# Kernel tuning notes

Hardware: AMD Instinct MI355X
Metric: run time of the kernel (lower is better)

Reference implementation:

```python
import jax, jax.numpy as jnp
import numpy as np
from jax import lax

B, S, H, I, E, K = 4, 4096, 1024, 3584, 8, 2


def setup_inputs() -> dict:
    key = jax.random.key(0)
    ks = jax.random.split(key, 5)
    scale_h = 1.0 / np.sqrt(H)
    scale_i = 1.0 / np.sqrt(I)
    return {
        "hidden_states": jax.random.normal(ks[0], (B, S, H), dtype=jnp.float32),
        "gate_w": jax.random.normal(ks[1], (E, H), dtype=jnp.float32) * scale_h,
        "w1": jax.random.normal(ks[2], (E, H, I), dtype=jnp.float32) * scale_h,
        "w3": jax.random.normal(ks[3], (E, H, I), dtype=jnp.float32) * scale_h,
        "w2": jax.random.normal(ks[4], (E, I, H), dtype=jnp.float32) * scale_i,
        "top_k": K,
    }


def reference(hidden_states, gate_w, w1, w3, w2, top_k):
    b, s, h = hidden_states.shape
    n_experts = gate_w.shape[0]
    x = hidden_states.reshape(-1, h)  # [T, H]

    # Router: softmax in fp32, top-k, renormalize (Mixtral style)
    logits = x @ gate_w.T  # [T, E]
    probs = jax.nn.softmax(logits.astype(jnp.float32), axis=-1)
    top_w, top_idx = lax.top_k(probs, top_k)  # [T, K]
    top_w = top_w.astype(x.dtype)
    top_w = top_w / jnp.sum(top_w, axis=-1, keepdims=True)

    # Per-token, per-expert combine weight: [T, E]
    one_hot = jax.nn.one_hot(top_idx, n_experts, dtype=x.dtype)  # [T, K, E]
    w_full = jnp.einsum("tk,tke->te", top_w, one_hot)

    out = jnp.zeros_like(x)
    for e in range(n_experts):  # fixed small loop over experts
        hidden = jax.nn.silu(x @ w1[e]) * (x @ w3[e])  # SwiGLU, [T, I]
        y = hidden @ w2[e]  # [T, H]
        out = out + y * w_full[:, e:e + 1]
    return out.reshape(b, s, h)
```

## Files before the change

kernel.cpp:

```cpp
#include <hip/hip_runtime.h>
#include <hip/hip_bf16.h>

#define T_TOK 16384
#define H_DIM 1024
#define I_DIM 3584
#define E_NUM 8
#define TOTP  32768

typedef __attribute__((ext_vector_type(8))) short s16x8;
typedef __attribute__((ext_vector_type(4))) float f32x4;
typedef unsigned short u16;

__device__ __forceinline__ u16 f2bf(float f) {
    union { float f; unsigned u; } c; c.f = f;
    unsigned r = c.u + 0x7fffu + ((c.u >> 16) & 1u);
    return (u16)(r >> 16);
}

__device__ __forceinline__ void glds16(const u16* g, u16* l) {
    __builtin_amdgcn_global_load_lds(
        (const __attribute__((address_space(1))) unsigned int*)g,
        (__attribute__((address_space(3))) unsigned int*)l,
        16, 0, 0);
}

__global__ __launch_bounds__(64)
void router_k(const float* __restrict__ x, const float* __restrict__ gw,
              int* __restrict__ tk_idx, float* __restrict__ tk_w,
              int* __restrict__ counts)
{
    int t = blockIdx.x;
    int lane = threadIdx.x;
    const float* xr = x + (size_t)t * H_DIM;
    float xv[16];
#pragma unroll
    for (int j = 0; j < 16; j++) xv[j] = xr[j * 64 + lane];
    float lg[E_NUM];
#pragma unroll
    for (int e = 0; e < E_NUM; e++) {
        const float* g = gw + e * H_DIM;
        float s = 0.f;
#pragma unroll
        for (int j = 0; j < 16; j++) s += xv[j] * g[j * 64 + lane];
#pragma unroll
        for (int off = 32; off > 0; off >>= 1) s += __shfl_xor(s, off, 64);
        lg[e] = s;
    }
    if (lane == 0) {
        int i1 = 0; float m1 = lg[0];
#pragma unroll
        for (int e = 1; e < E_NUM; e++) if (lg[e] > m1) { m1 = lg[e]; i1 = e; }
        int i2 = -1; float m2 = -3.4e38f;
#pragma unroll
        for (int e = 0; e < E_NUM; e++) if (e != i1 && lg[e] > m2) { m2 = lg[e]; i2 = e; }
        float p1 = 1.f / (1.f + __expf(m2 - m1));
        float p2 = 1.f - p1;
        tk_idx[t * 2]     = i1;
        tk_idx[t * 2 + 1] = i2;
        tk_w[t * 2]       = p1;
        tk_w[t * 2 + 1]   = p2;
        atomicAdd(&counts[i1], 1);
        atomicAdd(&counts[i2], 1);
    }
}

__global__ void offsets_k(const int* __restrict__ counts, int* __restrict__ offsets,
                          int* __restrict__ cursor)
{
    if (threadIdx.x == 0 && blockIdx.x == 0) {
        int acc = 0;
        for (int e = 0; e < E_NUM; e++) { offsets[e] = acc; cursor[e] = acc; acc += counts[e]; }
        offsets[E_NUM] = acc;
    }
}

__global__ __launch_bounds__(256)
void scatter_k(const int* __restrict__ tk_idx, const float* __restrict__ tk_w,
               int* __restrict__ cursor, int* __restrict__ perm, float* __restrict__ pw)
{
    int t = blockIdx.x * 256 + threadIdx.x;
    if (t >= T_TOK) return;
#pragma unroll
    for (int k = 0; k < 2; k++) {
        int e = tk_idx[t * 2 + k];
        int pos = atomicAdd(&cursor[e], 1);
        perm[pos] = t;
        pw[pos]   = tk_w[t * 2 + k];
    }
}

__global__ __launch_bounds__(256)
void cvt_x_k(const float* __restrict__ x, u16* __restrict__ xb)
{
    size_t i = ((size_t)blockIdx.x * 256 + threadIdx.x) * 8;
    float4 a = *reinterpret_cast<const float4*>(x + i);
    float4 b = *reinterpret_cast<const float4*>(x + i + 4);
    union { u16 s[8]; uint4 v; } u;
    u.s[0] = f2bf(a.x); u.s[1] = f2bf(a.y); u.s[2] = f2bf(a.z); u.s[3] = f2bf(a.w);
    u.s[4] = f2bf(b.x); u.s[5] = f2bf(b.y); u.s[6] = f2bf(b.z); u.s[7] = f2bf(b.w);
    *reinterpret_cast<uint4*>(xb + i) = u.v;
}

__global__ __launch_bounds__(256)
void tcvt_k(const float* __restrict__ src, u16* __restrict__ dst, int M, int N)
{
    size_t eo = (size_t)blockIdx.z * M * N;
    __shared__ u16 tl[32][33];
    int t = threadIdx.x;
    int r = t >> 3, c = (t & 7) * 4;
    int m0 = blockIdx.y * 32, n0 = blockIdx.x * 32;
    float4 v = *reinterpret_cast<const float4*>(src + eo + (size_t)(m0 + r) * N + n0 + c);
    tl[c + 0][r] = f2bf(v.x); tl[c + 1][r] = f2bf(v.y);
    tl[c + 2][r] = f2bf(v.z); tl[c + 3][r] = f2bf(v.w);
    __syncthreads();
    union { u16 s[4]; unsigned long long v; } u;
    u.s[0] = tl[r][c]; u.s[1] = tl[r][c + 1]; u.s[2] = tl[r][c + 2]; u.s[3] = tl[r][c + 3];
    *reinterpret_cast<unsigned long long*>(dst + eo + (size_t)(n0 + r) * M + m0 + c) = u.v;
}

__global__ __launch_bounds__(256, 2)
void gemm1_k(const u16* __restrict__ xb, const u16* __restrict__ w1t,
             const u16* __restrict__ w3t, const int* __restrict__ offsets,
             const int* __restrict__ perm, u16* __restrict__ hidden)
{
    int e = blockIdx.z;
    int base = offsets[e];
    int cnt  = offsets[e + 1] - base;
    int m0 = blockIdx.y * 128;
    if (m0 >= cnt) return;
    int n0 = blockIdx.x * 64;

    __shared__ u16 As[128 * 32];
    __shared__ u16 B1s[64 * 32];
    __shared__ u16 B3s[64 * 32];

    int t = threadIdx.x;
    int lane = t & 63, wave = t >> 6;
    int wm = (wave >> 1) * 64, wn = (wave & 1) * 32;
    int l15 = lane & 15, quad = lane >> 4;

    int sr = t >> 2;
    int sc = (t & 3) * 8;
    int p0 = m0 + sr;      if (p0 > cnt - 1) p0 = cnt - 1;
    int p1 = m0 + 64 + sr; if (p1 > cnt - 1) p1 = cnt - 1;
    const u16* a0p = xb + (size_t)perm[base + p0] * H_DIM + sc;
    const u16* a1p = xb + (size_t)perm[base + p1] * H_DIM + sc;
    const u16* b1p = w1t + (size_t)e * I_DIM * H_DIM + (size_t)(n0 + sr) * H_DIM + sc;
    const u16* b3p = w3t + (size_t)e * I_DIM * H_DIM + (size_t)(n0 + sr) * H_DIM + sc;

    u16* As0 = As + t * 8;
    u16* As1 = As + 2048 + t * 8;
    u16* B1d = B1s + t * 8;
    u16* B3d = B3s + t * 8;

    f32x4 acc1[4][2] = {};
    f32x4 acc3[4][2] = {};

    for (int k0 = 0; k0 < H_DIM; k0 += 32) {
        glds16(a0p + k0, As0);
        glds16(a1p + k0, As1);
        glds16(b1p + k0, B1d);
        glds16(b3p + k0, B3d);
        __syncthreads();
        s16x8 af[4];
#pragma unroll
        for (int i = 0; i < 4; i++)
            af[i] = *reinterpret_cast<const s16x8*>(As + (wm + i * 16 + l15) * 32 + quad * 8);
#pragma unroll
        for (int j = 0; j < 2; j++) {
            s16x8 b1 = *reinterpret_cast<const s16x8*>(B1s + (wn + j * 16 + l15) * 32 + quad * 8);
            s16x8 b3 = *reinterpret_cast<const s16x8*>(B3s + (wn + j * 16 + l15) * 32 + quad * 8);
#pragma unroll
            for (int i = 0; i < 4; i++) {
                acc1[i][j] = __builtin_amdgcn_mfma_f32_16x16x32_bf16(af[i], b1, acc1[i][j], 0, 0, 0);
                acc3[i][j] = __builtin_amdgcn_mfma_f32_16x16x32_bf16(af[i], b3, acc3[i][j], 0, 0, 0);
            }
        }
        __syncthreads();
    }

#pragma unroll
    for (int i = 0; i < 4; i++) {
#pragma unroll
        for (int j = 0; j < 2; j++) {
            int col = n0 + wn + j * 16 + l15;
#pragma unroll
            for (int r = 0; r < 4; r++) {
                int p = m0 + wm + i * 16 + quad * 4 + r;
                if (p < cnt) {
                    float z1 = acc1[i][j][r];
                    float z3 = acc3[i][j][r];
                    float hv = (z1 / (1.f + __expf(-z1))) * z3;
                    hidden[(size_t)(base + p) * I_DIM + col] = f2bf(hv);
                }
            }
        }
    }
}

__global__ __launch_bounds__(256, 2)
void gemm2_k(const u16* __restrict__ hidden, const u16* __restrict__ w2t,
             const int* __restrict__ offsets, const int* __restrict__ perm,
             const float* __restrict__ pw, float* __restrict__ out)
{
    int e = blockIdx.z;
    int base = offsets[e];
    int cnt  = offsets[e + 1] - base;
    int m0 = blockIdx.y * 128;
    if (m0 >= cnt) return;
    int n0 = blockIdx.x * 128;

    __shared__ u16 As[128 * 32];
    __shared__ u16 Bs[128 * 32];

    int t = threadIdx.x;
    int lane = t & 63, wave = t >> 6;
    int wm = (wave >> 1) * 64, wn = (wave & 1) * 64;
    int l15 = lane & 15, quad = lane >> 4;

    int sr = t >> 2;
    int sc = (t & 3) * 8;
    int p0 = m0 + sr;      if (p0 > cnt - 1) p0 = cnt - 1;
    int p1 = m0 + 64 + sr; if (p1 > cnt - 1) p1 = cnt - 1;
    const u16* a0p = hidden + (size_t)(base + p0) * I_DIM + sc;
    const u16* a1p = hidden + (size_t)(base + p1) * I_DIM + sc;
    const u16* wb  = w2t + (size_t)e * H_DIM * I_DIM;
    const u16* b0p = wb + (size_t)(n0 + sr) * I_DIM + sc;
    const u16* b1p = wb + (size_t)(n0 + 64 + sr) * I_DIM + sc;

    u16* As0 = As + t * 8;
    u16* As1 = As + 2048 + t * 8;
    u16* Bs0 = Bs + t * 8;
    u16* Bs1 = Bs + 2048 + t * 8;

    f32x4 acc[4][4] = {};

    for (int k0 = 0; k0 < I_DIM; k0 += 32) {
        glds16(a0p + k0, As0);
        glds16(a1p + k0, As1);
        glds16(b0p + k0, Bs0);
        glds16(b1p + k0, Bs1);
        __syncthreads();
        s16x8 af[4];
#pragma unroll
        for (int i = 0; i < 4; i++)
            af[i] = *reinterpret_cast<const s16x8*>(As + (wm + i * 16 + l15) * 32 + quad * 8);
#pragma unroll
        for (int j = 0; j < 4; j++) {
            s16x8 bfv = *reinterpret_cast<const s16x8*>(Bs + (wn + j * 16 + l15) * 32 + quad * 8);
#pragma unroll
            for (int i = 0; i < 4; i++)
                acc[i][j] = __builtin_amdgcn_mfma_f32_16x16x32_bf16(af[i], bfv, acc[i][j], 0, 0, 0);
        }
        __syncthreads();
    }

#pragma unroll
    for (int i = 0; i < 4; i++) {
#pragma unroll
        for (int r = 0; r < 4; r++) {
            int p = m0 + wm + i * 16 + quad * 4 + r;
            if (p < cnt) {
                int tok = perm[base + p];
                float wgt = pw[base + p];
                float* orow = out + (size_t)tok * H_DIM + n0 + wn;
#pragma unroll
                for (int j = 0; j < 4; j++)
                    atomicAdd(orow + j * 16 + l15, wgt * acc[i][j][r]);
            }
        }
    }
}

extern "C" void kernel_launch(void* const* d_in, const int* in_sizes, int n_in,
                              void* d_out, int out_size, void* d_ws, size_t ws_size,
                              hipStream_t stream)
{
    (void)in_sizes; (void)n_in; (void)ws_size;
    const float* x  = (const float*)d_in[0];
    const float* gw = (const float*)d_in[1];
    const float* w1 = (const float*)d_in[2];
    const float* w3 = (const float*)d_in[3];
    const float* w2 = (const float*)d_in[4];
    float* out = (float*)d_out;

    char* ws = (char*)d_ws;
    int*   counts  = (int*)ws;
    int*   offsets = counts + 8;
    int*   cursor  = offsets + 9;
    int*   tk_idx  = (int*)(ws + 128);
    float* tk_w    = (float*)(ws + 128 + 131072);
    int*   perm    = (int*)(ws + 128 + 2 * 131072);
    float* pw      = (float*)(ws + 128 + 3 * 131072);
    u16* xb     = (u16*)(ws + (1 << 20));
    u16* w1t    = xb + 16777216ull;
    u16* w3t    = w1t + 29360128ull;
    u16* w2t    = w3t + 29360128ull;
    u16* hidden = w2t + 29360128ull;

    hipMemsetAsync(ws, 0, 128, stream);
    router_k<<<T_TOK, 64, 0, stream>>>(x, gw, tk_idx, tk_w, counts);
    offsets_k<<<1, 64, 0, stream>>>(counts, offsets, cursor);
    scatter_k<<<T_TOK / 256, 256, 0, stream>>>(tk_idx, tk_w, cursor, perm, pw);
    cvt_x_k<<<8192, 256, 0, stream>>>(x, xb);
    tcvt_k<<<dim3(I_DIM / 32, H_DIM / 32, E_NUM), 256, 0, stream>>>(w1, w1t, H_DIM, I_DIM);
    tcvt_k<<<dim3(I_DIM / 32, H_DIM / 32, E_NUM), 256, 0, stream>>>(w3, w3t, H_DIM, I_DIM);
    tcvt_k<<<dim3(H_DIM / 32, I_DIM / 32, E_NUM), 256, 0, stream>>>(w2, w2t, I_DIM, H_DIM);
    gemm1_k<<<dim3(I_DIM / 64, 128, E_NUM), 256, 0, stream>>>(xb, w1t, w3t, offsets, perm, hidden);
    hipMemsetAsync(out, 0, (size_t)out_size * sizeof(float), stream);
    gemm2_k<<<dim3(H_DIM / 128, 128, E_NUM), 256, 0, stream>>>(hidden, w2t, offsets, perm, pw, out);
}
```

Baseline: 1.915 ms.

## Replace atomic output scatter with per-slot buffer and gather combine kernel

gemm2 now writes each routed row plainly into a per-slot fp32 buffer instead of doing atomicAdd into the output, and a new combine kernel sums the two slots per token using a position map recorded in scatter. The routing weight moves into the gemm1 epilogue, so it is applied before the bf16 rounding of hidden. The x-to-bf16 conversion is folded into the router kernel, and the output memset is dropped. The aim is to remove atomic contention and the extra launches, at the cost of a 128 MB intermediate buffer that reuses the xb region and an extra read/write pass.

After: 1.869 ms. 2.4% less time.

```diff
diff --git a/kernel.cpp b/kernel.cpp
--- a/kernel.cpp
+++ b/kernel.cpp
@@ -27,7 +27,7 @@
 __global__ __launch_bounds__(64)
 void router_k(const float* __restrict__ x, const float* __restrict__ gw,
               int* __restrict__ tk_idx, float* __restrict__ tk_w,
-              int* __restrict__ counts)
+              int* __restrict__ counts, u16* __restrict__ xb)
 {
     int t = blockIdx.x;
     int lane = threadIdx.x;
@@ -35,6 +35,9 @@
     float xv[16];
 #pragma unroll
     for (int j = 0; j < 16; j++) xv[j] = xr[j * 64 + lane];
+    u16* xo = xb + (size_t)t * H_DIM;
+#pragma unroll
+    for (int j = 0; j < 16; j++) xo[j * 64 + lane] = f2bf(xv[j]);
     float lg[E_NUM];
 #pragma unroll
     for (int e = 0; e < E_NUM; e++) {
@@ -76,7 +79,8 @@
 
 __global__ __launch_bounds__(256)
 void scatter_k(const int* __restrict__ tk_idx, const float* __restrict__ tk_w,
-               int* __restrict__ cursor, int* __restrict__ perm, float* __restrict__ pw)
+               int* __restrict__ cursor, int* __restrict__ perm, float* __restrict__ pw,
+               int* __restrict__ posmap)
 {
     int t = blockIdx.x * 256 + threadIdx.x;
     if (t >= T_TOK) return;
@@ -86,19 +90,8 @@
         int pos = atomicAdd(&cursor[e], 1);
         perm[pos] = t;
         pw[pos]   = tk_w[t * 2 + k];
-    }
-}
-
-__global__ __launch_bounds__(256)
-void cvt_x_k(const float* __restrict__ x, u16* __restrict__ xb)
-{
-    size_t i = ((size_t)blockIdx.x * 256 + threadIdx.x) * 8;
-    float4 a = *reinterpret_cast<const float4*>(x + i);
-    float4 b = *reinterpret_cast<const float4*>(x + i + 4);
-    union { u16 s[8]; uint4 v; } u;
-    u.s[0] = f2bf(a.x); u.s[1] = f2bf(a.y); u.s[2] = f2bf(a.z); u.s[3] = f2bf(a.w);
-    u.s[4] = f2bf(b.x); u.s[5] = f2bf(b.y); u.s[6] = f2bf(b.z); u.s[7] = f2bf(b.w);
-    *reinterpret_cast<uint4*>(xb + i) = u.v;
+        posmap[t * 2 + k] = pos;
+    }
 }
 
 __global__ __launch_bounds__(256)
@@ -121,7 +114,8 @@
 __global__ __launch_bounds__(256, 2)
 void gemm1_k(const u16* __restrict__ xb, const u16* __restrict__ w1t,
              const u16* __restrict__ w3t, const int* __restrict__ offsets,
-             const int* __restrict__ perm, u16* __restrict__ hidden)
+             const int* __restrict__ perm, const float* __restrict__ pw,
+             u16* __restrict__ hidden)
 {
     int e = blockIdx.z;
     int base = offsets[e];
@@ -190,7 +184,7 @@
                 if (p < cnt) {
                     float z1 = acc1[i][j][r];
                     float z3 = acc3[i][j][r];
-                    float hv = (z1 / (1.f + __expf(-z1))) * z3;
+                    float hv = (z1 / (1.f + __expf(-z1))) * z3 * pw[base + p];
                     hidden[(size_t)(base + p) * I_DIM + col] = f2bf(hv);
                 }
             }
@@ -200,8 +194,7 @@
 
 __global__ __launch_bounds__(256, 2)
 void gemm2_k(const u16* __restrict__ hidden, const u16* __restrict__ w2t,
-             const int* __restrict__ offsets, const int* __restrict__ perm,
-             const float* __restrict__ pw, float* __restrict__ out)
+             const int* __restrict__ offsets, float* __restrict__ ybuf)
 {
     int e = blockIdx.z;
     int base = offsets[e];
@@ -261,22 +254,34 @@
         for (int r = 0; r < 4; r++) {
             int p = m0 + wm + i * 16 + quad * 4 + r;
             if (p < cnt) {
-                int tok = perm[base + p];
-                float wgt = pw[base + p];
-                float* orow = out + (size_t)tok * H_DIM + n0 + wn;
+                float* orow = ybuf + (size_t)(base + p) * H_DIM + n0 + wn;
 #pragma unroll
                 for (int j = 0; j < 4; j++)
-                    atomicAdd(orow + j * 16 + l15, wgt * acc[i][j][r]);
+                    orow[j * 16 + l15] = acc[i][j][r];
             }
         }
     }
+}
+
+__global__ __launch_bounds__(256)
+void combine_k(const float* __restrict__ ybuf, const int* __restrict__ posmap,
+               float* __restrict__ out)
+{
+    int t = blockIdx.x;
+    int c = threadIdx.x * 4;
+    int pa = posmap[t * 2];
+    int pb = posmap[t * 2 + 1];
+    float4 a = *reinterpret_cast<const float4*>(ybuf + (size_t)pa * H_DIM + c);
+    float4 b = *reinterpret_cast<const float4*>(ybuf + (size_t)pb * H_DIM + c);
+    float4 o = make_float4(a.x + b.x, a.y + b.y, a.z + b.z, a.w + b.w);
+    *reinterpret_cast<float4*>(out + (size_t)t * H_DIM + c) = o;
 }
 
 extern "C" void kernel_launch(void* const* d_in, const int* in_sizes, int n_in,
                               void* d_out, int out_size, void* d_ws, size_t ws_size,
                               hipStream_t stream)
 {
-    (void)in_sizes; (void)n_in; (void)ws_size;
+    (void)in_sizes; (void)n_in; (void)ws_size; (void)out_size;
     const float* x  = (const float*)d_in[0];
     const float* gw = (const float*)d_in[1];
     const float* w1 = (const float*)d_in[2];
@@ -292,21 +297,22 @@
     float* tk_w    = (float*)(ws + 128 + 131072);
     int*   perm    = (int*)(ws + 128 + 2 * 131072);
     float* pw      = (float*)(ws + 128 + 3 * 131072);
+    int*   posmap  = (int*)(ws + 128 + 4 * 131072);
     u16* xb     = (u16*)(ws + (1 << 20));
     u16* w1t    = xb + 16777216ull;
     u16* w3t    = w1t + 29360128ull;
     u16* w2t    = w3t + 29360128ull;
     u16* hidden = w2t + 29360128ull;
+    float* ybuf = (float*)(ws + (1 << 20));
 
     hipMemsetAsync(ws, 0, 128, stream);
-    router_k<<<T_TOK, 64, 0, stream>>>(x, gw, tk_idx, tk_w, counts);
+    router_k<<<T_TOK, 64, 0, stream>>>(x, gw, tk_idx, tk_w, counts, xb);
     offsets_k<<<1, 64, 0, stream>>>(counts, offsets, cursor);
-    scatter_k<<<T_TOK / 256, 256, 0, stream>>>(tk_idx, tk_w, cursor, perm, pw);
-    cvt_x_k<<<8192, 256, 0, stream>>>(x, xb);
+    scatter_k<<<T_TOK / 256, 256, 0, stream>>>(tk_idx, tk_w, cursor, perm, pw, posmap);
     tcvt_k<<<dim3(I_DIM / 32, H_DIM / 32, E_NUM), 256, 0, stream>>>(w1, w1t, H_DIM, I_DIM);
     tcvt_k<<<dim3(I_DIM / 32, H_DIM / 32, E_NUM), 256, 0, stream>>>(w3, w3t, H_DIM, I_DIM);
     tcvt_k<<<dim3(H_DIM / 32, I_DIM / 32, E_NUM), 256, 0, stream>>>(w2, w2t, I_DIM, H_DIM);
-    gemm1_k<<<dim3(I_DIM / 64, 128, E_NUM), 256, 0, stream>>>(xb, w1t, w3t, offsets, perm, hidden);
-    hipMemsetAsync(out, 0, (size_t)out_size * sizeof(float), stream);
-    gemm2_k<<<dim3(H_DIM / 128, 128, E_NUM), 256, 0, stream>>>(hidden, w2t, offsets, perm, pw, out);
-}
+    gemm1_k<<<dim3(I_DIM / 64, 128, E_NUM), 256, 0, stream>>>(xb, w1t, w3t, offsets, perm, pw, hidden);
+    gemm2_k<<<dim3(H_DIM / 128, 128, E_NUM), 256, 0, stream>>>(hidden, w2t, offsets, ybuf);
+    combine_k<<<T_TOK, 256, 0, stream>>>(ybuf, posmap, out);
+}
```
